# Kernel optimization log

Hardware: AMD Instinct MI355X
Metric: run time of the kernel (lower is better)

The kernel has to match this reference:

```python
import jax, jax.numpy as jnp
import numpy as np

B, P, J, MOT, K, NB, WN, H = 64, 12273, 80, 94, 64, 20, 17, 128
W_POSE = 1.0

def euler_to_rotmat(a):
    # a: [..., 3] radians, R = Rz @ Ry @ Rx
    sx, sy, sz = jnp.sin(a[..., 0]), jnp.sin(a[..., 1]), jnp.sin(a[..., 2])
    cx, cy, cz = jnp.cos(a[..., 0]), jnp.cos(a[..., 1]), jnp.cos(a[..., 2])
    r00 = cz * cy; r01 = cz * sy * sx - sz * cx; r02 = cz * sy * cx + sz * sx
    r10 = sz * cy; r11 = sz * sy * sx + cz * cx; r12 = sz * sy * cx - cz * sx
    r20 = -sy;     r21 = cy * sx;                r22 = cy * cx
    return jnp.stack([jnp.stack([r00, r01, r02], -1),
                      jnp.stack([r10, r11, r12], -1),
                      jnp.stack([r20, r21, r22], -1)], -2)

def setup_inputs() -> dict:
    key = jax.random.key(0)
    ks = jax.random.split(key, 20)
    f32 = jnp.float32
    return {
        'in_pc_batch': jax.random.normal(ks[0], (B, P, 3), f32),
        't_nor': jax.random.normal(ks[1], (B, P, 3), f32),
        'rest_verts': jax.random.normal(ks[2], (P, 3), f32),
        'skin_weights': jax.random.uniform(ks[3], (P, J), f32),
        'mul_weight_list': jax.random.normal(ks[4], (J, MOT), f32),
        'query': jax.random.normal(ks[5], (B, J, 3), f32),
        'cloth_pose_std': jax.random.uniform(ks[6], (3,), f32),
        'cloth_pose_mean': jax.random.normal(ks[7], (3,), f32),
        'cloth_trans_std': jax.random.uniform(ks[8], (3,), f32),
        'cloth_trans_mean': jax.random.normal(ks[9], (3,), f32),
        'W1': jax.random.normal(ks[10], (3 + K, H), f32) * 0.1,
        'b1': jnp.zeros((H,), f32),
        'W2': jax.random.normal(ks[11], (H, 6), f32) * 0.1,
        'b2': jnp.zeros((6,), f32),
        'tmtemp': jax.random.normal(ks[12], (B, MOT, K), f32),
        'Wd': jax.random.normal(ks[13], (MOT * K, NB * WN), f32) * 0.02,
        'bd': jnp.zeros((NB * WN,), f32),
        'DPSD': jax.random.normal(ks[14], (NB, WN, P, 3), f32) * 0.1,
        'ssdr_res_std': jax.random.uniform(ks[15], (3,), f32),
        'ssdr_res_mean': jax.random.normal(ks[16], (3,), f32),
    }

def reference(in_pc_batch, t_nor, rest_verts, skin_weights, mul_weight_list,
              query, cloth_pose_std, cloth_pose_mean, cloth_trans_std,
              cloth_trans_mean, W1, b1, W2, b2, tmtemp, Wd, bd, DPSD,
              ssdr_res_std, ssdr_res_mean):
    # per-joint field input: [B, J, K]
    field_input = jnp.einsum('bjk,lj->blk', tmtemp, jax.nn.relu(mul_weight_list))
    # FieldNet: per-joint MLP on concat(query, field_input) -> [B, J, 6]
    h = jnp.concatenate([query, field_input], axis=-1)
    pred_rt = jax.nn.relu(h @ W1 + b1) @ W2 + b2
    pred_pose = pred_rt[..., 0:3] * cloth_pose_std + cloth_pose_mean
    pred_trans = (query + pred_rt[..., 3:6]) * cloth_trans_std + cloth_trans_mean
    # detailsnet + fused 20-basis accumulation: [B, P, 3]
    nbat = tmtemp.shape[0]
    detailkey = (tmtemp.reshape(nbat, -1) @ Wd + bd).reshape(nbat, NB, WN)
    detail_res = jnp.einsum('bnw,nwpx->bpx', detailkey, DPSD)
    detail_res = detail_res * ssdr_res_std + ssdr_res_mean
    # SSDR LBS skinning with Euler-angle rotations (degrees -> radians)
    R = euler_to_rotmat(jnp.deg2rad(pred_pose))            # [B, J, 3, 3]
    skinned = (jnp.einsum('pj,bjxy,py->bpx', skin_weights, R, rest_verts)
               + jnp.einsum('pj,bjx->bpx', skin_weights, pred_trans))
    out_pc = skinned + detail_res                          # [B, P, 3]
    loss_pose_l1 = jnp.mean(jnp.abs(in_pc_batch[:, :, 0:3] - out_pc))
    loss = loss_pose_l1 * W_POSE + 1e-4 * jnp.mean(DPSD ** 2)
    return loss[None], out_pc
```

## Files before the change

kernel.cpp:

```cpp
#include <hip/hip_runtime.h>

#define B_   64
#define P_   12273
#define J_   80
#define MOT_ 94
#define K_   64
#define H_   128
#define Q_   340
#define NE_  36819
#define MK_  6016
#define PW_  12288
#define STG_ 2356416

typedef float v4f  __attribute__((ext_vector_type(4)));
typedef float v8f  __attribute__((ext_vector_type(8)));
typedef float v16f __attribute__((ext_vector_type(16)));
#define AS4 __attribute__((address_space(4)))

__device__ __forceinline__ const AS4 float* unif(const float* p){
  return (const AS4 float*)(unsigned long long)p;
}
__device__ __forceinline__ const AS4 v4f* univ4(const float* p){
  return (const AS4 v4f*)(unsigned long long)p;
}
__device__ __forceinline__ const AS4 v16f* univ16(const float* p){
  return (const AS4 v16f*)(unsigned long long)p;
}

__global__ __launch_bounds__(256) void k_tmt(
    const float* __restrict__ tm, float* __restrict__ tm_t)
{
  __shared__ float smem[64 * 65];
  int t = threadIdx.x;
  int m0 = blockIdx.x * 64;
  int ml = t & 63, g = t >> 6;
  #pragma unroll
  for (int r = 0; r < 16; r++){
    int b = g * 16 + r;
    smem[ml * 65 + b] = tm[(size_t)b * MK_ + m0 + ml];
  }
  __syncthreads();
  int bl = t & 63;
  #pragma unroll
  for (int r = 0; r < 16; r++){
    int m = g * 16 + r;
    tm_t[(size_t)(m0 + m) * 64 + bl] = smem[m * 65 + bl];
  }
}

__global__ __launch_bounds__(256) void k_main(
    const float* __restrict__ query, const float* __restrict__ mwl,
    const float* __restrict__ tm,    const float* __restrict__ W1,
    const float* __restrict__ b1,    const float* __restrict__ W2,
    const float* __restrict__ b2,    const float* __restrict__ cps,
    const float* __restrict__ cpm,   const float* __restrict__ cts,
    const float* __restrict__ ctm,   const float* __restrict__ skin,
    const float* __restrict__ tm_t,  const float* __restrict__ Wd,
    float* __restrict__ G,           float* __restrict__ part,
    float* __restrict__ w_t,         float* __restrict__ lacc)
{
  __shared__ float smem[80 * 65];
  int blk = blockIdx.x;
  int t = threadIdx.x;
  if (blk < 564){
    int lane = t & 63;
    int wid = __builtin_amdgcn_readfirstlane(t >> 6);
    int qt = blk % 6;
    int my = blk / 6;
    int q = qt * 64 + lane;
    bool vq = q < Q_;
    int m0 = my * 64;
    const AS4 v16f* tr = univ16(tm_t);
    float acc[16];
    #pragma unroll
    for (int i = 0; i < 16; i++) acc[i] = 0.f;
    float wbuf[4];
    #pragma unroll
    for (int i = 0; i < 4; i++)
      wbuf[i] = vq ? Wd[(size_t)(m0 + i) * Q_ + q] : 0.f;
    v16f tb0 = tr[(size_t)(m0 + 0) * 4 + wid];
    v16f tb1 = tr[(size_t)(m0 + 1) * 4 + wid];
    #pragma unroll 4
    for (int mm = 0; mm < 60; mm++){
      float wd = wbuf[mm & 3];
      wbuf[mm & 3] = vq ? Wd[(size_t)(m0 + mm + 4) * Q_ + q] : 0.f;
      v16f tv = tb0; tb0 = tb1;
      tb1 = tr[(size_t)(m0 + mm + 2) * 4 + wid];
      #pragma unroll
      for (int i = 0; i < 16; i++) acc[i] = fmaf(tv[i], wd, acc[i]);
    }
    #pragma unroll
    for (int mm = 60; mm < 64; mm++){
      float wd = wbuf[mm & 3];
      v16f tv = tb0; tb0 = tb1;
      if (mm < 62) tb1 = tr[(size_t)(m0 + mm + 2) * 4 + wid];
      #pragma unroll
      for (int i = 0; i < 16; i++) acc[i] = fmaf(tv[i], wd, acc[i]);
    }
    float* pb = part + ((size_t)my * 6 + qt) * 4096 + (size_t)(wid * 16) * 64;
    #pragma unroll
    for (int i = 0; i < 16; i++) pb[i * 64 + lane] = acc[i];
  } else if (blk < 1844){
    int lane = t & 63;
    int wid = __builtin_amdgcn_readfirstlane(t >> 6);
    int bj = (blk - 564) * 4 + wid;
    int b = bj / J_, l = bj - b * J_;
    float* hs = smem + wid * 80;
    float acc = 0.f;
    const AS4 float* mp = unif(mwl + l * MOT_);
    const float* tp = tm + (size_t)b * MK_ + lane;
    #pragma unroll 2
    for (int j = 0; j < MOT_; j++){
      float w = mp[j]; w = w > 0.f ? w : 0.f;
      acc = fmaf(w, tp[j * K_], acc);
    }
    hs[3 + lane] = acc;
    if (lane < 3) hs[lane] = query[(size_t)bj * 3 + lane];
    __syncthreads();
    float a1 = b1[lane], a2 = b1[lane + 64];
    for (int i = 0; i < 3 + K_; i++){
      float hv = hs[i];
      a1 = fmaf(hv, W1[i * H_ + lane], a1);
      a2 = fmaf(hv, W1[i * H_ + 64 + lane], a2);
    }
    a1 = a1 > 0.f ? a1 : 0.f;
    a2 = a2 > 0.f ? a2 : 0.f;
    const AS4 float* b2c = unif(b2);
    float rt[6];
    #pragma unroll
    for (int o = 0; o < 6; o++){
      float po = fmaf(a1, W2[lane * 6 + o], a2 * W2[(lane + 64) * 6 + o]);
      #pragma unroll
      for (int off = 32; off; off >>= 1) po += __shfl_xor(po, off);
      rt[o] = po + b2c[o];
    }
    const float D2R = 0.017453292519943295f;
    float ax = fmaf(rt[0], cps[0], cpm[0]) * D2R;
    float ay = fmaf(rt[1], cps[1], cpm[1]) * D2R;
    float az = fmaf(rt[2], cps[2], cpm[2]) * D2R;
    float tx = fmaf(hs[0] + rt[3], cts[0], ctm[0]);
    float ty = fmaf(hs[1] + rt[4], cts[1], ctm[1]);
    float tz = fmaf(hs[2] + rt[5], cts[2], ctm[2]);
    float sx, cx, sy, cy, sz, cz;
    sincosf(ax, &sx, &cx); sincosf(ay, &sy, &cy); sincosf(az, &sz, &cz);
    if (lane == 0){
      float4 r0 = make_float4(cz*cy, cz*sy*sx - sz*cx, cz*sy*cx + sz*sx, tx);
      float4 r1 = make_float4(sz*cy, sz*sy*sx + cz*cx, sz*sy*cx - cz*sx, ty);
      float4 r2 = make_float4(-sy,   cy*sx,            cy*cx,            tz);
      float4* g = (float4*)(G + (size_t)bj * 12);
      g[0] = r0; g[1] = r1; g[2] = r2;
    }
  } else if (blk < 2036){
    int p0 = (blk - 1844) * 64;
    #pragma unroll
    for (int k = 0; k < 20; k++){
      int idx = k * 256 + t;
      int pl = idx / 80, j = idx - pl * 80;
      int p = p0 + pl;
      smem[j * 65 + pl] = (p < P_) ? skin[(size_t)p * J_ + j] : 0.f;
    }
    __syncthreads();
    #pragma unroll
    for (int k = 0; k < 20; k++){
      int idx = k * 256 + t;
      int j = idx >> 6, pl = idx & 63;
      w_t[(size_t)j * PW_ + p0 + pl] = smem[j * 65 + pl];
    }
  } else {
    if (t < 2) lacc[t] = 0.f;
  }
}

__global__ __launch_bounds__(256) void k_dkred(
    const float* __restrict__ part, const float* __restrict__ bd,
    float* __restrict__ dk_t, int S)
{
  int t = threadIdx.x;
  int jj = blockIdx.x * 32 + (t >> 3);
  int dl = t & 7;
  int b = jj / Q_, q = jj - b * Q_;
  int qt = q >> 6, ql = q & 63;
  const float* pp = part + (size_t)qt * 4096 + b * 64 + ql;
  float s = 0.f;
  for (int d = dl; d < S; d += 8) s += pp[(size_t)d * 6 * 4096];
  s += __shfl_xor(s, 1); s += __shfl_xor(s, 2); s += __shfl_xor(s, 4);
  if (dl == 0) dk_t[q * 64 + b] = bd[q] + s;
}

__device__ __forceinline__ void dk_consume(const AS4 v16f* dkv, int qa, int wid,
                                           const float* dc, float* acc,
                                           float& sq, bool doSq)
{
  v16f r0 = dkv[(qa + 0) * 4 + wid];
  v16f r1 = dkv[(qa + 1) * 4 + wid];
  v16f r2 = dkv[(qa + 2) * 4 + wid];
  v16f r3 = dkv[(qa + 3) * 4 + wid];
  v16f r4 = dkv[(qa + 4) * 4 + wid];
  if (doSq){
    #pragma unroll
    for (int i = 0; i < 5; i++) sq = fmaf(dc[i], dc[i], sq);
  }
  #pragma unroll
  for (int i = 0; i < 16; i++){
    acc[i] = fmaf(r0[i], dc[0], acc[i]);
    acc[i] = fmaf(r1[i], dc[1], acc[i]);
    acc[i] = fmaf(r2[i], dc[2], acc[i]);
    acc[i] = fmaf(r3[i], dc[3], acc[i]);
    acc[i] = fmaf(r4[i], dc[4], acc[i]);
  }
}

__global__ __launch_bounds__(256) void k_detail(
    const float* __restrict__ DPSD, const float* __restrict__ dk_t,
    float* __restrict__ stg, float* __restrict__ out,
    float* __restrict__ lacc, int QSTEP)
{
  int t = threadIdx.x;
  int lane = t & 63;
  int wid = __builtin_amdgcn_readfirstlane(t >> 6);
  int b0 = wid * 16;
  int e = blockIdx.x * 64 + lane;
  bool ve = e < NE_;
  int q0 = blockIdx.y * QSTEP;
  int qn = Q_ - q0; if (qn > QSTEP) qn = QSTEP;
  const AS4 v16f* dkv = univ16(dk_t);
  const float* Dp = DPSD + (ve ? e : 0);
  float acc[16];
  #pragma unroll
  for (int i = 0; i < 16; i++) acc[i] = 0.f;
  float sq = 0.f;
  bool doSq = (wid == 0);
  int ng = qn / 5;
  float da[5], db[5];
  #pragma unroll
  for (int i = 0; i < 5; i++) da[i] = Dp[(size_t)(q0 + i) * NE_];
  #pragma unroll
  for (int i = 0; i < 5; i++) db[i] = Dp[(size_t)(q0 + 5 + i) * NE_];
  for (int g = 0; g + 2 < ng; g += 2){
    int qa = q0 + g * 5;
    float ta[5], tb[5];
    #pragma unroll
    for (int i = 0; i < 5; i++) ta[i] = Dp[(size_t)(qa + 10 + i) * NE_];
    dk_consume(dkv, qa, wid, da, acc, sq, doSq);
    #pragma unroll
    for (int i = 0; i < 5; i++) da[i] = ta[i];
    #pragma unroll
    for (int i = 0; i < 5; i++) tb[i] = Dp[(size_t)(qa + 15 + i) * NE_];
    dk_consume(dkv, qa + 5, wid, db, acc, sq, doSq);
    #pragma unroll
    for (int i = 0; i < 5; i++) db[i] = tb[i];
  }
  dk_consume(dkv, q0 + (ng - 2) * 5, wid, da, acc, sq, doSq);
  dk_consume(dkv, q0 + (ng - 1) * 5, wid, db, acc, sq, doSq);
  if (ve){
    bool toOut = (blockIdx.y + 1 == gridDim.y);
    float* dst = toOut ? (out + 1 + e) : (stg + (size_t)blockIdx.y * STG_ + e);
    #pragma unroll
    for (int i = 0; i < 16; i++)
      dst[(size_t)(b0 + i) * NE_] = acc[i];
  }
  if (doSq){
    if (!ve) sq = 0.f;
    #pragma unroll
    for (int off = 32; off; off >>= 1) sq += __shfl_xor(sq, off);
    if (lane == 0) atomicAdd(&lacc[1], sq);
  }
}

__global__ __launch_bounds__(256) void k_skin(
    const float* __restrict__ G, const float* __restrict__ w_t,
    const float* __restrict__ rest, const float* __restrict__ in_pc,
    const float* __restrict__ stg, const float* __restrict__ rstd,
    const float* __restrict__ rmean,
    float* __restrict__ out, float* __restrict__ lacc, int nst)
{
  int t = threadIdx.x;
  int lane = t & 63;
  int wid = __builtin_amdgcn_readfirstlane(t >> 6);
  int p  = blockIdx.x * 64 + lane;
  int bA = blockIdx.y * 8 + wid * 2;
  const AS4 v4f* gA = univ4(G + (size_t)bA * J_ * 12);
  const AS4 v4f* gB = univ4(G + ((size_t)bA + 1) * J_ * 12);
  float accA[12], accB[12];
  #pragma unroll
  for (int c = 0; c < 12; c++){ accA[c] = 0.f; accB[c] = 0.f; }
  const float* wp = w_t + p;
  #pragma unroll 4
  for (int j = 0; j < J_; j++){
    float w = wp[(size_t)j * PW_];
    v4f a0 = gA[j * 3 + 0], a1 = gA[j * 3 + 1], a2 = gA[j * 3 + 2];
    v4f c0 = gB[j * 3 + 0], c1 = gB[j * 3 + 1], c2 = gB[j * 3 + 2];
    #pragma unroll
    for (int c = 0; c < 4; c++){
      accA[c]     = fmaf(w, a0[c], accA[c]);
      accA[4 + c] = fmaf(w, a1[c], accA[4 + c]);
      accA[8 + c] = fmaf(w, a2[c], accA[8 + c]);
      accB[c]     = fmaf(w, c0[c], accB[c]);
      accB[4 + c] = fmaf(w, c1[c], accB[4 + c]);
      accB[8 + c] = fmaf(w, c2[c], accB[8 + c]);
    }
  }
  bool vp = p < P_;
  float vx = 0.f, vy = 0.f, vz = 0.f;
  if (vp){ vx = rest[p * 3]; vy = rest[p * 3 + 1]; vz = rest[p * 3 + 2]; }
  float srs[3], srm[3];
  #pragma unroll
  for (int x = 0; x < 3; x++){ srs[x] = rstd[x]; srm[x] = rmean[x]; }
  float lsum = 0.f;
  if (vp){
    size_t baseA = ((size_t)bA * P_ + p) * 3;
    size_t baseB = baseA + (size_t)P_ * 3;
    #pragma unroll
    for (int x = 0; x < 3; x++){
      float det = out[1 + baseA + x];
      for (int s = 0; s < nst; s++) det += stg[(size_t)s * STG_ + baseA + x];
      float v = fmaf(accA[x*4+0], vx, fmaf(accA[x*4+1], vy, fmaf(accA[x*4+2], vz, accA[x*4+3])));
      v += fmaf(det, srs[x], srm[x]);
      lsum += fabsf(in_pc[baseA + x] - v);
      out[1 + baseA + x] = v;
    }
    #pragma unroll
    for (int x = 0; x < 3; x++){
      float det = out[1 + baseB + x];
      for (int s = 0; s < nst; s++) det += stg[(size_t)s * STG_ + baseB + x];
      float v = fmaf(accB[x*4+0], vx, fmaf(accB[x*4+1], vy, fmaf(accB[x*4+2], vz, accB[x*4+3])));
      v += fmaf(det, srs[x], srm[x]);
      lsum += fabsf(in_pc[baseB + x] - v);
      out[1 + baseB + x] = v;
    }
  }
  #pragma unroll
  for (int off = 32; off; off >>= 1) lsum += __shfl_xor(lsum, off);
  __shared__ float red[4];
  if (lane == 0) red[wid] = lsum;
  __syncthreads();
  if (t == 0) atomicAdd(&lacc[0], red[0] + red[1] + red[2] + red[3]);
}

__global__ void k_finalize(const float* __restrict__ lacc, float* __restrict__ out){
  if (threadIdx.x == 0 && blockIdx.x == 0){
    float loss = lacc[0] * (1.f / 2356416.f) + 1e-4f * (lacc[1] * (1.f / 12518460.f));
    out[0] = loss;
  }
}

extern "C" void kernel_launch(void* const* d_in, const int* in_sizes, int n_in,
                              void* d_out, int out_size, void* d_ws, size_t ws_size,
                              hipStream_t stream){
  const float* in_pc = (const float*)d_in[0];
  const float* rest  = (const float*)d_in[2];
  const float* skin  = (const float*)d_in[3];
  const float* mwl   = (const float*)d_in[4];
  const float* query = (const float*)d_in[5];
  const float* cps   = (const float*)d_in[6];
  const float* cpm   = (const float*)d_in[7];
  const float* cts   = (const float*)d_in[8];
  const float* ctm   = (const float*)d_in[9];
  const float* W1    = (const float*)d_in[10];
  const float* b1    = (const float*)d_in[11];
  const float* W2    = (const float*)d_in[12];
  const float* b2    = (const float*)d_in[13];
  const float* tm    = (const float*)d_in[14];
  const float* Wd    = (const float*)d_in[15];
  const float* bd    = (const float*)d_in[16];
  const float* DPSD  = (const float*)d_in[17];
  const float* rstd  = (const float*)d_in[18];
  const float* rmean = (const float*)d_in[19];
  float* out = (float*)d_out;

  float* ws   = (float*)d_ws;
  float* G    = ws;
  float* dk_t = G + 61440;
  float* lacc = dk_t + 21760;
  float* tm_t = lacc + 64;
  float* w_t  = tm_t + 385024;
  float* un   = w_t + 983040;

  size_t have = ws_size / 4;
  const size_t base = 1451328;
  int nqh = (have >= base + (size_t)STG_) ? 2 : 1;
  int QSTEP = Q_ / nqh;

  k_tmt     <<<94, 256, 0, stream>>>(tm, tm_t);
  k_main    <<<2037, 256, 0, stream>>>(query, mwl, tm, W1, b1, W2, b2,
                                       cps, cpm, cts, ctm, skin,
                                       tm_t, Wd, G, un, w_t, lacc);
  k_dkred   <<<680, 256, 0, stream>>>(un, bd, dk_t, 94);
  k_detail  <<<dim3(576, nqh), 256, 0, stream>>>(DPSD, dk_t, un, out, lacc, QSTEP);
  k_skin    <<<dim3(192, 8), 256, 0, stream>>>(G, w_t, rest, in_pc, un, rstd, rmean,
                                               out, lacc, nqh - 1);
  k_finalize<<<1, 64, 0, stream>>>(lacc, out);
}
```

Measured before the change: 252.7 us.

## Fuse tmtemp transpose into GEMM blocks via LDS and finalize loss in last block

Removes the separate transpose kernel: each Wd-GEMM block now loads its 64x64 tmtemp tile into shared memory with a padded stride and reads it as vec4 from LDS. The standalone finalize kernel is also dropped; the last k_skin block, detected with an atomic counter in lacc[2], computes the loss. Together these remove two kernel launches and the global round trip for tm_t. The cost is an extra __syncthreads and LDS traffic in the GEMM blocks, plus a hardcoded block count (1536) in the completion check.

```diff
diff --git a/kernel.cpp b/kernel.cpp
--- a/kernel.cpp
+++ b/kernel.cpp
@@ -13,7 +13,6 @@
 #define STG_ 2356416
 
 typedef float v4f  __attribute__((ext_vector_type(4)));
-typedef float v8f  __attribute__((ext_vector_type(8)));
 typedef float v16f __attribute__((ext_vector_type(16)));
 #define AS4 __attribute__((address_space(4)))
 
@@ -25,27 +24,6 @@
 }
 __device__ __forceinline__ const AS4 v16f* univ16(const float* p){
   return (const AS4 v16f*)(unsigned long long)p;
-}
-
-__global__ __launch_bounds__(256) void k_tmt(
-    const float* __restrict__ tm, float* __restrict__ tm_t)
-{
-  __shared__ float smem[64 * 65];
-  int t = threadIdx.x;
-  int m0 = blockIdx.x * 64;
-  int ml = t & 63, g = t >> 6;
-  #pragma unroll
-  for (int r = 0; r < 16; r++){
-    int b = g * 16 + r;
-    smem[ml * 65 + b] = tm[(size_t)b * MK_ + m0 + ml];
-  }
-  __syncthreads();
-  int bl = t & 63;
-  #pragma unroll
-  for (int r = 0; r < 16; r++){
-    int m = g * 16 + r;
-    tm_t[(size_t)(m0 + m) * 64 + bl] = smem[m * 65 + bl];
-  }
 }
 
 __global__ __launch_bounds__(256) void k_main(
@@ -55,7 +33,7 @@
     const float* __restrict__ b2,    const float* __restrict__ cps,
     const float* __restrict__ cpm,   const float* __restrict__ cts,
     const float* __restrict__ ctm,   const float* __restrict__ skin,
-    const float* __restrict__ tm_t,  const float* __restrict__ Wd,
+    const float* __restrict__ Wd,
     float* __restrict__ G,           float* __restrict__ part,
     float* __restrict__ w_t,         float* __restrict__ lacc)
 {
@@ -70,7 +48,13 @@
     int q = qt * 64 + lane;
     bool vq = q < Q_;
     int m0 = my * 64;
-    const AS4 v16f* tr = univ16(tm_t);
+    #pragma unroll
+    for (int r = 0; r < 16; r++){
+      int b = wid * 16 + r;
+      smem[lane * 72 + b] = tm[(size_t)b * MK_ + m0 + lane];
+    }
+    __syncthreads();
+    const v4f* sr = (const v4f*)smem;
     float acc[16];
     #pragma unroll
     for (int i = 0; i < 16; i++) acc[i] = 0.f;
@@ -78,24 +62,19 @@
     #pragma unroll
     for (int i = 0; i < 4; i++)
       wbuf[i] = vq ? Wd[(size_t)(m0 + i) * Q_ + q] : 0.f;
-    v16f tb0 = tr[(size_t)(m0 + 0) * 4 + wid];
-    v16f tb1 = tr[(size_t)(m0 + 1) * 4 + wid];
     #pragma unroll 4
-    for (int mm = 0; mm < 60; mm++){
+    for (int mm = 0; mm < 64; mm++){
       float wd = wbuf[mm & 3];
-      wbuf[mm & 3] = vq ? Wd[(size_t)(m0 + mm + 4) * Q_ + q] : 0.f;
-      v16f tv = tb0; tb0 = tb1;
-      tb1 = tr[(size_t)(m0 + mm + 2) * 4 + wid];
+      if (mm + 4 < 64) wbuf[mm & 3] = vq ? Wd[(size_t)(m0 + mm + 4) * Q_ + q] : 0.f;
+      int rb = mm * 18 + wid * 4;
+      v4f t0 = sr[rb], t1 = sr[rb + 1], t2 = sr[rb + 2], t3 = sr[rb + 3];
       #pragma unroll
-      for (int i = 0; i < 16; i++) acc[i] = fmaf(tv[i], wd, acc[i]);
-    }
-    #pragma unroll
-    for (int mm = 60; mm < 64; mm++){
-      float wd = wbuf[mm & 3];
-      v16f tv = tb0; tb0 = tb1;
-      if (mm < 62) tb1 = tr[(size_t)(m0 + mm + 2) * 4 + wid];
-      #pragma unroll
-      for (int i = 0; i < 16; i++) acc[i] = fmaf(tv[i], wd, acc[i]);
+      for (int c = 0; c < 4; c++){
+        acc[c]      = fmaf(t0[c], wd, acc[c]);
+        acc[4 + c]  = fmaf(t1[c], wd, acc[4 + c]);
+        acc[8 + c]  = fmaf(t2[c], wd, acc[8 + c]);
+        acc[12 + c] = fmaf(t3[c], wd, acc[12 + c]);
+      }
     }
     float* pb = part + ((size_t)my * 6 + qt) * 4096 + (size_t)(wid * 16) * 64;
     #pragma unroll
@@ -167,7 +146,7 @@
       w_t[(size_t)j * PW_ + p0 + pl] = smem[j * 65 + pl];
     }
   } else {
-    if (t < 2) lacc[t] = 0.f;
+    if (t < 3) lacc[t] = 0.f;
   }
 }
 
@@ -334,13 +313,16 @@
   __shared__ float red[4];
   if (lane == 0) red[wid] = lsum;
   __syncthreads();
-  if (t == 0) atomicAdd(&lacc[0], red[0] + red[1] + red[2] + red[3]);
-}
-
-__global__ void k_finalize(const float* __restrict__ lacc, float* __restrict__ out){
-  if (threadIdx.x == 0 && blockIdx.x == 0){
-    float loss = lacc[0] * (1.f / 2356416.f) + 1e-4f * (lacc[1] * (1.f / 12518460.f));
-    out[0] = loss;
+  if (t == 0){
+    atomicAdd(&lacc[0], red[0] + red[1] + red[2] + red[3]);
+    __threadfence();
+    unsigned prev = atomicAdd((unsigned int*)(lacc + 2), 1u);
+    if (prev == 1535u){
+      __threadfence();
+      float l0 = atomicAdd(&lacc[0], 0.f);
+      float l1 = atomicAdd(&lacc[1], 0.f);
+      out[0] = l0 * (1.f / 2356416.f) + 1e-4f * (l1 * (1.f / 12518460.f));
+    }
   }
 }
 
@@ -381,13 +363,11 @@
   int nqh = (have >= base + (size_t)STG_) ? 2 : 1;
   int QSTEP = Q_ / nqh;
 
-  k_tmt     <<<94, 256, 0, stream>>>(tm, tm_t);
   k_main    <<<2037, 256, 0, stream>>>(query, mwl, tm, W1, b1, W2, b2,
-                                       cps, cpm, cts, ctm, skin,
-                                       tm_t, Wd, G, un, w_t, lacc);
+                                       cps, cpm, cts, ctm, skin, Wd,
+                                       G, un, w_t, lacc);
   k_dkred   <<<680, 256, 0, stream>>>(un, bd, dk_t, 94);
   k_detail  <<<dim3(576, nqh), 256, 0, stream>>>(DPSD, dk_t, un, out, lacc, QSTEP);
   k_skin    <<<dim3(192, 8), 256, 0, stream>>>(G, w_t, rest, in_pc, un, rstd, rmean,
                                                out, lacc, nqh - 1);
-  k_finalize<<<1, 64, 0, stream>>>(lacc, out);
-}
+}
```

Result: slower. 312.5 us (+23.7%).
